# Performance work log

Measured on AMD Instinct MI355X. Metric: run time of the kernel, lower is better.

## Reference

```python
import jax, jax.numpy as jnp
import numpy as np

HIDDEN = 2048
VOCAB = 50257


def setup_inputs() -> dict:
    key = jax.random.key(0)
    ks = jax.random.split(key, 9)
    s = 1.0 / np.sqrt(HIDDEN)
    return {
        "input": jax.random.randint(ks[0], (1,), 0, VOCAB, dtype=jnp.int64) if jax.config.jax_enable_x64 else jax.random.randint(ks[0], (1,), 0, VOCAB, dtype=jnp.int32),
        "hidden": jax.random.normal(ks[1], (1, 1, HIDDEN), dtype=jnp.float32),
        "embedding": jax.random.normal(ks[2], (VOCAB, HIDDEN), dtype=jnp.float32),
        "w_ih": jax.random.uniform(ks[3], (3 * HIDDEN, HIDDEN), jnp.float32, -s, s),
        "w_hh": jax.random.uniform(ks[4], (3 * HIDDEN, HIDDEN), jnp.float32, -s, s),
        "b_ih": jax.random.uniform(ks[5], (3 * HIDDEN,), jnp.float32, -s, s),
        "b_hh": jax.random.uniform(ks[6], (3 * HIDDEN,), jnp.float32, -s, s),
        "out_w": jax.random.uniform(ks[7], (VOCAB, HIDDEN), jnp.float32, -s, s),
        "out_b": jax.random.uniform(ks[8], (VOCAB,), jnp.float32, -s, s),
    }


def reference(input, hidden, embedding, w_ih, w_hh, b_ih, b_hh, out_w, out_b):
    # embedding lookup + view(1,1,-1) + relu  -> x: [H]
    x = jax.nn.relu(embedding[input[0]])
    h = hidden[0, 0]  # [H]
    # PyTorch GRU single step: gates ordered (r, z, n)
    gi = w_ih @ x + b_ih  # [3H]
    gh = w_hh @ h + b_hh  # [3H]
    i_r, i_z, i_n = jnp.split(gi, 3)
    h_r, h_z, h_n = jnp.split(gh, 3)
    r = jax.nn.sigmoid(i_r + h_r)
    z = jax.nn.sigmoid(i_z + h_z)
    n = jnp.tanh(i_n + r * h_n)
    h_new = (1.0 - z) * n + z * h  # [H]
    # output projection (nn.Linear: x @ W.T + b) + log_softmax(dim=1)
    logits = out_w @ h_new + out_b  # [V]
    logp = jax.nn.log_softmax(logits)[None, :]  # [1, V]
    return logp, h_new[None, None, :]
```

## Files before the change

### kernel.cpp

```cpp
#include <hip/hip_runtime.h>
#include <math.h>

#define H 2048
#define V 50257

#define LOGITS_BLOCKS 2048
#define LOGITS_WAVES (LOGITS_BLOCKS * 4)
#define FIN_BLOCKS 52

__device__ __forceinline__ float wave_reduce_sum(float v) {
#pragma unroll
    for (int off = 32; off > 0; off >>= 1)
        v += __shfl_down(v, off, 64);
    return v;
}

__global__ __launch_bounds__(384) void k_gru(
    const int* __restrict__ idx_p,
    const float* __restrict__ emb,
    const float* __restrict__ hid,
    const float* __restrict__ w_ih, const float* __restrict__ w_hh,
    const float* __restrict__ b_ih, const float* __restrict__ b_hh,
    float* __restrict__ hnew_ws, float* __restrict__ hnew_out) {
    __shared__ float xs[H];
    __shared__ float hs[H];
    __shared__ float partial[6][2];
    int tid = threadIdx.x;

    long idx = (long)idx_p[0];
    const float4* embrow = (const float4*)(emb + idx * (long)H);
    for (int i = tid; i < H / 4; i += 384) {
        float4 e = embrow[i];
        e.x = fmaxf(e.x, 0.f); e.y = fmaxf(e.y, 0.f);
        e.z = fmaxf(e.z, 0.f); e.w = fmaxf(e.w, 0.f);
        ((float4*)xs)[i] = e;
        ((float4*)hs)[i] = ((const float4*)hid)[i];
    }
    __syncthreads();

    int wid = tid >> 6, lane = tid & 63;
    int gate = wid % 3;
    const float* W   = (wid < 3) ? w_ih : w_hh;
    const float* vec = (wid < 3) ? xs : hs;
    int j0 = blockIdx.x;
    int j1 = blockIdx.x + 1024;
    const float4* r0 = (const float4*)(W + ((size_t)gate * H + j0) * (size_t)H);
    const float4* r1 = (const float4*)(W + ((size_t)gate * H + j1) * (size_t)H);

    float4 vreg[8];
#pragma unroll
    for (int it = 0; it < 8; ++it)
        vreg[it] = ((const float4*)vec)[it * 64 + lane];

    float a0 = 0.f, a1 = 0.f;
#pragma unroll
    for (int it = 0; it < 8; ++it) {
        float4 wa = r0[it * 64 + lane];
        float4 wb = r1[it * 64 + lane];
        a0 += wa.x * vreg[it].x + wa.y * vreg[it].y + wa.z * vreg[it].z + wa.w * vreg[it].w;
        a1 += wb.x * vreg[it].x + wb.y * vreg[it].y + wb.z * vreg[it].z + wb.w * vreg[it].w;
    }
    a0 = wave_reduce_sum(a0);
    a1 = wave_reduce_sum(a1);
    if (lane == 0) { partial[wid][0] = a0; partial[wid][1] = a1; }
    __syncthreads();

    if (tid < 2) {
        int j = (tid == 0) ? j0 : j1;
        float i_r = partial[0][tid] + b_ih[j];
        float i_z = partial[1][tid] + b_ih[H + j];
        float i_n = partial[2][tid] + b_ih[2 * H + j];
        float h_r = partial[3][tid] + b_hh[j];
        float h_z = partial[4][tid] + b_hh[H + j];
        float h_n = partial[5][tid] + b_hh[2 * H + j];
        float r = 1.f / (1.f + expf(-(i_r + h_r)));
        float z = 1.f / (1.f + expf(-(i_z + h_z)));
        float n = tanhf(i_n + r * h_n);
        float hv = (1.f - z) * n + z * hs[j];
        hnew_ws[j] = hv;
        hnew_out[j] = hv;
    }
}

__global__ __launch_bounds__(256) void k_logits(
    const float* __restrict__ out_w, const float* __restrict__ out_b,
    const float* __restrict__ hnew,
    float* __restrict__ logits, float2* __restrict__ partials) {
    __shared__ float hs[H];
    __shared__ float pm[4], ps[4];
    int tid = threadIdx.x;
    for (int i = tid; i < H / 4; i += 256)
        ((float4*)hs)[i] = ((const float4*)hnew)[i];
    __syncthreads();

    int wid = tid >> 6, lane = tid & 63;
    float4 vreg[8];
#pragma unroll
    for (int it = 0; it < 8; ++it)
        vreg[it] = ((const float4*)hs)[it * 64 + lane];

    float m = -INFINITY, s = 0.f;
    for (int r = blockIdx.x * 4 + wid; r < V; r += LOGITS_WAVES) {
        const float4* row = (const float4*)(out_w + (size_t)r * (size_t)H);
        float acc = 0.f;
#pragma unroll
        for (int it = 0; it < 8; ++it) {
            float4 w4 = row[it * 64 + lane];
            acc += w4.x * vreg[it].x + w4.y * vreg[it].y + w4.z * vreg[it].z + w4.w * vreg[it].w;
        }
        acc = wave_reduce_sum(acc);
        if (lane == 0) {
            float l = acc + out_b[r];
            logits[r] = l;
            float M = fmaxf(m, l);
            s = s * __expf(m - M) + __expf(l - M);
            m = M;
        }
    }
    if (lane == 0) { pm[wid] = m; ps[wid] = s; }
    __syncthreads();
    if (tid == 0) {
        float M = fmaxf(fmaxf(pm[0], pm[1]), fmaxf(pm[2], pm[3]));
        float S = ps[0] * __expf(pm[0] - M) + ps[1] * __expf(pm[1] - M) +
                  ps[2] * __expf(pm[2] - M) + ps[3] * __expf(pm[3] - M);
        partials[blockIdx.x] = make_float2(M, S);
    }
}

__global__ __launch_bounds__(256) void k_finalize(
    const float* __restrict__ logits, const float2* __restrict__ partials,
    float* __restrict__ out) {
    __shared__ float pm[4], ps[4];
    __shared__ float cs;
    int tid = threadIdx.x;

    float m = -INFINITY, s = 0.f;
    for (int i = tid; i < LOGITS_BLOCKS; i += 256) {
        float2 p = partials[i];
        float M = fmaxf(m, p.x);
        s = s * __expf(m - M) + p.y * __expf(p.x - M);
        m = M;
    }
#pragma unroll
    for (int off = 32; off > 0; off >>= 1) {
        float om = __shfl_down(m, off, 64);
        float os = __shfl_down(s, off, 64);
        float M = fmaxf(m, om);
        s = s * __expf(m - M) + os * __expf(om - M);
        m = M;
    }
    int wid = tid >> 6, lane = tid & 63;
    if (lane == 0) { pm[wid] = m; ps[wid] = s; }
    __syncthreads();
    if (tid == 0) {
        float M = fmaxf(fmaxf(pm[0], pm[1]), fmaxf(pm[2], pm[3]));
        float S = ps[0] * __expf(pm[0] - M) + ps[1] * __expf(pm[1] - M) +
                  ps[2] * __expf(pm[2] - M) + ps[3] * __expf(pm[3] - M);
        cs = M + logf(S);
    }
    __syncthreads();
    float C = cs;

    int gid = blockIdx.x * 256 + tid;
    const int nf = V / 4;
    for (int i = gid; i < nf; i += FIN_BLOCKS * 256) {
        float4 l4 = ((const float4*)logits)[i];
        l4.x -= C; l4.y -= C; l4.z -= C; l4.w -= C;
        ((float4*)out)[i] = l4;
    }
    if (gid == 0) {
        for (int i = nf * 4; i < V; ++i) out[i] = logits[i] - C;
    }
}

extern "C" void kernel_launch(void* const* d_in, const int* in_sizes, int n_in,
                              void* d_out, int out_size, void* d_ws, size_t ws_size,
                              hipStream_t stream) {
    const int*   idx    = (const int*)d_in[0];
    const float* hidden = (const float*)d_in[1];
    const float* emb    = (const float*)d_in[2];
    const float* w_ih   = (const float*)d_in[3];
    const float* w_hh   = (const float*)d_in[4];
    const float* b_ih   = (const float*)d_in[5];
    const float* b_hh   = (const float*)d_in[6];
    const float* out_w  = (const float*)d_in[7];
    const float* out_b  = (const float*)d_in[8];

    float* out = (float*)d_out;
    float* ws  = (float*)d_ws;
    float*  hnew     = ws;
    float*  logits   = ws + H;
    float2* partials = (float2*)(ws + H + ((V + 1) & ~1));

    k_gru<<<1024, 384, 0, stream>>>(idx, emb, hidden, w_ih, w_hh, b_ih, b_hh,
                                    hnew, out + V);
    k_logits<<<LOGITS_BLOCKS, 256, 0, stream>>>(out_w, out_b, hnew, logits, partials);
    k_finalize<<<FIN_BLOCKS, 256, 0, stream>>>(logits, partials, out);
}
```

Before: 100.0 us.

## Fuse GRU, logits and log-softmax into one cooperative persistent kernel

Replaces the three-kernel sequence with a single cooperative kernel that uses grid-wide syncs between the gate GEMV, the pointwise GRU update plus logits GEMV, and the log-softmax finalize. Every block recomputes the full h_new from gate pre-activations held in global scratch. Logits are written straight to the output and normalized in place, which removes the separate logits buffer. Launch overhead and inter-kernel gaps are meant to go away, in exchange for grid.sync costs, a grid limited by occupancy (at most 1024 blocks) and redundant per-block GRU pointwise work. A fallback to the old kernels is kept if the cooperative launch fails.

```diff
diff --git a/kernel.cpp b/kernel.cpp
--- a/kernel.cpp
+++ b/kernel.cpp
@@ -1,11 +1,13 @@
 #include <hip/hip_runtime.h>
+#include <hip/hip_cooperative_groups.h>
 #include <math.h>
+
+namespace cg = cooperative_groups;
 
 #define H 2048
 #define V 50257
-
+#define NTHR 256
 #define LOGITS_BLOCKS 2048
-#define LOGITS_WAVES (LOGITS_BLOCKS * 4)
 #define FIN_BLOCKS 52
 
 __device__ __forceinline__ float wave_reduce_sum(float v) {
@@ -15,9 +17,176 @@
     return v;
 }
 
-__global__ __launch_bounds__(384) void k_gru(
-    const int* __restrict__ idx_p,
-    const float* __restrict__ emb,
+__global__ __launch_bounds__(NTHR, 4) void k_fused(
+    const int* __restrict__ idx_p, const float* __restrict__ emb,
+    const float* __restrict__ hid,
+    const float* __restrict__ w_ih, const float* __restrict__ w_hh,
+    const float* __restrict__ b_ih, const float* __restrict__ b_hh,
+    const float* __restrict__ out_w, const float* __restrict__ out_b,
+    float* __restrict__ out, float* __restrict__ gscratch,
+    float2* __restrict__ partials) {
+    cg::grid_group grid = cg::this_grid();
+    __shared__ float xs[H];
+    __shared__ float hs[H];
+    __shared__ float pm[4], ps[4];
+    __shared__ float cs;
+    const int tid = threadIdx.x, wid = tid >> 6, lane = tid & 63;
+    const int nblk = gridDim.x;
+    const int nw = nblk * 4;
+    const int gw = blockIdx.x * 4 + wid;
+
+    long idx = (long)idx_p[0];
+    const float4* er = (const float4*)(emb + idx * (long)H);
+    for (int i = tid; i < H / 4; i += NTHR) {
+        float4 e = er[i];
+        e.x = fmaxf(e.x, 0.f); e.y = fmaxf(e.y, 0.f);
+        e.z = fmaxf(e.z, 0.f); e.w = fmaxf(e.w, 0.f);
+        ((float4*)xs)[i] = e;
+        ((float4*)hs)[i] = ((const float4*)hid)[i];
+    }
+    __syncthreads();
+
+    for (int r = gw; r < 6 * H; r += nw) {
+        const float* W   = (r < 3 * H) ? (w_ih + (size_t)r * H)
+                                       : (w_hh + (size_t)(r - 3 * H) * H);
+        const float* vec = (r < 3 * H) ? xs : hs;
+        float acc = 0.f;
+#pragma unroll
+        for (int it = 0; it < 8; ++it) {
+            float4 w4 = ((const float4*)W)[it * 64 + lane];
+            float4 v4 = ((const float4*)vec)[it * 64 + lane];
+            acc += w4.x * v4.x + w4.y * v4.y + w4.z * v4.z + w4.w * v4.w;
+        }
+        acc = wave_reduce_sum(acc);
+        if (lane == 0) gscratch[r] = acc;
+    }
+    grid.sync();
+
+    const float4* gs4 = (const float4*)gscratch;
+    const float4* bi4 = (const float4*)b_ih;
+    const float4* bh4 = (const float4*)b_hh;
+    for (int q = tid; q < H / 4; q += NTHR) {
+        float4 ir = gs4[q],        iz = gs4[512 + q],  in_ = gs4[1024 + q];
+        float4 hr = gs4[1536 + q], hz = gs4[2048 + q], hn  = gs4[2560 + q];
+        float4 br = bi4[q],        bz = bi4[512 + q],  bn  = bi4[1024 + q];
+        float4 cr = bh4[q],        cz = bh4[512 + q],  cn  = bh4[1024 + q];
+        float4 h4 = ((const float4*)hs)[q];
+        float irv[4] = {ir.x + br.x, ir.y + br.y, ir.z + br.z, ir.w + br.w};
+        float izv[4] = {iz.x + bz.x, iz.y + bz.y, iz.z + bz.z, iz.w + bz.w};
+        float inv[4] = {in_.x + bn.x, in_.y + bn.y, in_.z + bn.z, in_.w + bn.w};
+        float hrv[4] = {hr.x + cr.x, hr.y + cr.y, hr.z + cr.z, hr.w + cr.w};
+        float hzv[4] = {hz.x + cz.x, hz.y + cz.y, hz.z + cz.z, hz.w + cz.w};
+        float hnv[4] = {hn.x + cn.x, hn.y + cn.y, hn.z + cn.z, hn.w + cn.w};
+        float hov[4] = {h4.x, h4.y, h4.z, h4.w};
+        float hv[4];
+#pragma unroll
+        for (int c = 0; c < 4; ++c) {
+            float r = 1.f / (1.f + __expf(-(irv[c] + hrv[c])));
+            float z = 1.f / (1.f + __expf(-(izv[c] + hzv[c])));
+            float n = tanhf(inv[c] + r * hnv[c]);
+            hv[c] = (1.f - z) * n + z * hov[c];
+        }
+        ((float4*)xs)[q] = make_float4(hv[0], hv[1], hv[2], hv[3]);
+        if (blockIdx.x == 0) {
+#pragma unroll
+            for (int c = 0; c < 4; ++c) out[V + 4 * q + c] = hv[c];
+        }
+    }
+    __syncthreads();
+
+    float4 vreg[8];
+#pragma unroll
+    for (int it = 0; it < 8; ++it)
+        vreg[it] = ((const float4*)xs)[it * 64 + lane];
+
+    float m = -INFINITY, s = 0.f;
+    for (int r0 = gw; r0 < V; r0 += 2 * nw) {
+        int r1 = r0 + nw;
+        if (r1 < V) {
+            const float4* row0 = (const float4*)(out_w + (size_t)r0 * H);
+            const float4* row1 = (const float4*)(out_w + (size_t)r1 * H);
+            float a0 = 0.f, a1 = 0.f;
+#pragma unroll
+            for (int it = 0; it < 8; ++it) {
+                float4 wa = row0[it * 64 + lane];
+                float4 wb = row1[it * 64 + lane];
+                a0 += wa.x * vreg[it].x + wa.y * vreg[it].y + wa.z * vreg[it].z + wa.w * vreg[it].w;
+                a1 += wb.x * vreg[it].x + wb.y * vreg[it].y + wb.z * vreg[it].z + wb.w * vreg[it].w;
+            }
+            a0 = wave_reduce_sum(a0);
+            a1 = wave_reduce_sum(a1);
+            if (lane == 0) {
+                float l0 = a0 + out_b[r0], l1 = a1 + out_b[r1];
+                out[r0] = l0; out[r1] = l1;
+                float M = fmaxf(m, fmaxf(l0, l1));
+                s = s * __expf(m - M) + __expf(l0 - M) + __expf(l1 - M);
+                m = M;
+            }
+        } else {
+            const float4* row0 = (const float4*)(out_w + (size_t)r0 * H);
+            float a0 = 0.f;
+#pragma unroll
+            for (int it = 0; it < 8; ++it) {
+                float4 wa = row0[it * 64 + lane];
+                a0 += wa.x * vreg[it].x + wa.y * vreg[it].y + wa.z * vreg[it].z + wa.w * vreg[it].w;
+            }
+            a0 = wave_reduce_sum(a0);
+            if (lane == 0) {
+                float l0 = a0 + out_b[r0];
+                out[r0] = l0;
+                float M = fmaxf(m, l0);
+                s = s * __expf(m - M) + __expf(l0 - M);
+                m = M;
+            }
+        }
+    }
+    if (lane == 0) { pm[wid] = m; ps[wid] = s; }
+    __syncthreads();
+    if (tid == 0) {
+        float M = fmaxf(fmaxf(pm[0], pm[1]), fmaxf(pm[2], pm[3]));
+        float S = ps[0] * __expf(pm[0] - M) + ps[1] * __expf(pm[1] - M) +
+                  ps[2] * __expf(pm[2] - M) + ps[3] * __expf(pm[3] - M);
+        partials[blockIdx.x] = make_float2(M, S);
+    }
+    grid.sync();
+
+    {
+        float mm = -INFINITY, ss = 0.f;
+        for (int i = tid; i < nblk; i += NTHR) {
+            float2 p = partials[i];
+            float M = fmaxf(mm, p.x);
+            ss = ss * __expf(mm - M) + p.y * __expf(p.x - M);
+            mm = M;
+        }
+#pragma unroll
+        for (int off = 32; off > 0; off >>= 1) {
+            float om = __shfl_down(mm, off, 64);
+            float os = __shfl_down(ss, off, 64);
+            float M = fmaxf(mm, om);
+            ss = ss * __expf(mm - M) + os * __expf(om - M);
+            mm = M;
+        }
+        if (lane == 0) { pm[wid] = mm; ps[wid] = ss; }
+        __syncthreads();
+        if (tid == 0) {
+            float M = fmaxf(fmaxf(pm[0], pm[1]), fmaxf(pm[2], pm[3]));
+            float S = ps[0] * __expf(pm[0] - M) + ps[1] * __expf(pm[1] - M) +
+                      ps[2] * __expf(pm[2] - M) + ps[3] * __expf(pm[3] - M);
+            cs = M + logf(S);
+        }
+        __syncthreads();
+    }
+    float C = cs;
+    for (int g = blockIdx.x * NTHR + tid; g < V / 4; g += nblk * NTHR) {
+        float4 l4 = ((const float4*)out)[g];
+        l4.x -= C; l4.y -= C; l4.z -= C; l4.w -= C;
+        ((float4*)out)[g] = l4;
+    }
+    if (blockIdx.x == 0 && tid == 0) out[V - 1] -= C;
+}
+
+__global__ __launch_bounds__(384) void k_gru_fb(
+    const int* __restrict__ idx_p, const float* __restrict__ emb,
     const float* __restrict__ hid,
     const float* __restrict__ w_ih, const float* __restrict__ w_hh,
     const float* __restrict__ b_ih, const float* __restrict__ b_hh,
@@ -26,7 +195,6 @@
     __shared__ float hs[H];
     __shared__ float partial[6][2];
     int tid = threadIdx.x;
-
     long idx = (long)idx_p[0];
     const float4* embrow = (const float4*)(emb + idx * (long)H);
     for (int i = tid; i < H / 4; i += 384) {
@@ -37,21 +205,16 @@
         ((float4*)hs)[i] = ((const float4*)hid)[i];
     }
     __syncthreads();
-
     int wid = tid >> 6, lane = tid & 63;
     int gate = wid % 3;
     const float* W   = (wid < 3) ? w_ih : w_hh;
     const float* vec = (wid < 3) ? xs : hs;
-    int j0 = blockIdx.x;
-    int j1 = blockIdx.x + 1024;
+    int j0 = blockIdx.x, j1 = blockIdx.x + 1024;
     const float4* r0 = (const float4*)(W + ((size_t)gate * H + j0) * (size_t)H);
     const float4* r1 = (const float4*)(W + ((size_t)gate * H + j1) * (size_t)H);
-
     float4 vreg[8];
 #pragma unroll
-    for (int it = 0; it < 8; ++it)
-        vreg[it] = ((const float4*)vec)[it * 64 + lane];
-
+    for (int it = 0; it < 8; ++it) vreg[it] = ((const float4*)vec)[it * 64 + lane];
     float a0 = 0.f, a1 = 0.f;
 #pragma unroll
     for (int it = 0; it < 8; ++it) {
@@ -64,7 +227,6 @@
     a1 = wave_reduce_sum(a1);
     if (lane == 0) { partial[wid][0] = a0; partial[wid][1] = a1; }
     __syncthreads();
-
     if (tid < 2) {
         int j = (tid == 0) ? j0 : j1;
         float i_r = partial[0][tid] + b_ih[j];
@@ -82,25 +244,22 @@
     }
 }
 
-__global__ __launch_bounds__(256) void k_logits(
+__global__ __launch_bounds__(256) void k_logits_fb(
     const float* __restrict__ out_w, const float* __restrict__ out_b,
     const float* __restrict__ hnew,
     float* __restrict__ logits, float2* __restrict__ partials) {
-    __shared__ float hs[H];
+    __shared__ float hsm[H];
     __shared__ float pm[4], ps[4];
     int tid = threadIdx.x;
     for (int i = tid; i < H / 4; i += 256)
-        ((float4*)hs)[i] = ((const float4*)hnew)[i];
-    __syncthreads();
-
+        ((float4*)hsm)[i] = ((const float4*)hnew)[i];
+    __syncthreads();
     int wid = tid >> 6, lane = tid & 63;
     float4 vreg[8];
 #pragma unroll
-    for (int it = 0; it < 8; ++it)
-        vreg[it] = ((const float4*)hs)[it * 64 + lane];
-
+    for (int it = 0; it < 8; ++it) vreg[it] = ((const float4*)hsm)[it * 64 + lane];
     float m = -INFINITY, s = 0.f;
-    for (int r = blockIdx.x * 4 + wid; r < V; r += LOGITS_WAVES) {
+    for (int r = blockIdx.x * 4 + wid; r < V; r += LOGITS_BLOCKS * 4) {
         const float4* row = (const float4*)(out_w + (size_t)r * (size_t)H);
         float acc = 0.f;
 #pragma unroll
@@ -127,13 +286,12 @@
     }
 }
 
-__global__ __launch_bounds__(256) void k_finalize(
+__global__ __launch_bounds__(256) void k_finalize_fb(
     const float* __restrict__ logits, const float2* __restrict__ partials,
     float* __restrict__ out) {
     __shared__ float pm[4], ps[4];
     __shared__ float cs;
     int tid = threadIdx.x;
-
     float m = -INFINITY, s = 0.f;
     for (int i = tid; i < LOGITS_BLOCKS; i += 256) {
         float2 p = partials[i];
@@ -160,7 +318,6 @@
     }
     __syncthreads();
     float C = cs;
-
     int gid = blockIdx.x * 256 + tid;
     const int nf = V / 4;
     for (int i = gid; i < nf; i += FIN_BLOCKS * 256) {
@@ -188,12 +345,41 @@
 
     float* out = (float*)d_out;
     float* ws  = (float*)d_ws;
+    float*  gscratch = ws;
+    float2* cpart    = (float2*)(ws + 6 * H);
+
+    int dev = 0;
+    (void)hipGetDevice(&dev);
+    int cus = 0;
+    (void)hipDeviceGetAttribute(&cus, hipDeviceAttributeMultiprocessorCount, dev);
+    int maxPerCU = 0;
+    hipError_t oe = hipOccupancyMaxActiveBlocksPerMultiprocessor(
+        &maxPerCU, (const void*)k_fused, NTHR, 0);
+
+    int nblk = 0;
+    if (oe == hipSuccess && cus > 0 && maxPerCU > 0) {
+        nblk = maxPerCU * cus;
+        if (nblk > 1024) nblk = 1024;
+    }
+
+    if (nblk >= 128) {
+        void* args[] = {
+            (void*)&idx, (void*)&emb, (void*)&hidden,
+            (void*)&w_ih, (void*)&w_hh, (void*)&b_ih, (void*)&b_hh,
+            (void*)&out_w, (void*)&out_b,
+            (void*)&out, (void*)&gscratch, (void*)&cpart,
+        };
+        hipError_t le = hipLaunchCooperativeKernel(
+            (const void*)k_fused, dim3(nblk), dim3(NTHR), args, 0, stream);
+        if (le == hipSuccess) return;
+    }
+
     float*  hnew     = ws;
     float*  logits   = ws + H;
     float2* partials = (float2*)(ws + H + ((V + 1) & ~1));
-
-    k_gru<<<1024, 384, 0, stream>>>(idx, emb, hidden, w_ih, w_hh, b_ih, b_hh,
-                                    hnew, out + V);
-    k_logits<<<LOGITS_BLOCKS, 256, 0, stream>>>(out_w, out_b, hnew, logits, partials);
-    k_finalize<<<FIN_BLOCKS, 256, 0, stream>>>(logits, partials, out);
-}
+    k_gru_fb<<<1024, 384, 0, stream>>>(idx, emb, hidden, w_ih, w_hh, b_ih, b_hh,
+                                       hnew, out + V);
+    k_logits_fb<<<LOGITS_BLOCKS, 256, 0, stream>>>(out_w, out_b, hnew, logits,
+                                                   partials);
+    k_finalize_fb<<<FIN_BLOCKS, 256, 0, stream>>>(logits, partials, out);
+}
```

Measured after the change: 217.4 us. 2.17x slower.
